# Performance work log

Hardware: AMD Instinct MI355X
Metric: run time of the kernel (lower is better)

The kernel has to match this reference:

```python
import jax, jax.numpy as jnp
import numpy as np

NEG_SLOPE = 0.01  # nn.LeakyReLU default

def leaky_relu(x):
    return jnp.where(x >= 0, x, NEG_SLOPE * x)

def rgcn_conv(x, weight, root, bias, src, dst, edge_type, num_relations, num_nodes):
    """PyG RGCNConv with default mean aggregation.
    weight: [R, in, out], root: [in, out], bias: [out].
    out[i] = x[i] @ root + bias + sum_r mean_{edges e of type r with dst=i} (x[src_e] @ W_r)
    """
    out = x @ root + bias
    for r in range(num_relations):
        mask = (edge_type == r)
        h = x @ weight[r]                       # [N, out] transform once per relation
        msg = h[src] * mask[:, None].astype(x.dtype)   # [E, out], zeroed off-relation
        s = jax.ops.segment_sum(msg, dst, num_segments=num_nodes)
        cnt = jax.ops.segment_sum(mask.astype(x.dtype), dst, num_segments=num_nodes)
        out = out + s / jnp.maximum(cnt, 1.0)[:, None]
    return out

def setup_inputs() -> dict:
    key = jax.random.key(0)
    ks = jax.random.split(key, 16)
    N, E, IN, HID, OUT, R = 50000, 800000, 768, 256, 2, 2
    x = jax.random.normal(ks[0], (N, IN), dtype=jnp.float32)
    edge_index = jax.random.randint(ks[1], (2, E), 0, N, dtype=jnp.int64)
    edge_weight = jax.random.uniform(ks[2], (E,), dtype=jnp.float32)
    edge_type = jax.random.randint(ks[3], (E,), 0, R, dtype=jnp.int64)
    def lin(k, fin, fout):
        s = 1.0 / np.sqrt(fin)
        k1, k2 = jax.random.split(k)
        W = jax.random.uniform(k1, (fin, fout), minval=-s, maxval=s, dtype=jnp.float32)
        b = jax.random.uniform(k2, (fout,), minval=-s, maxval=s, dtype=jnp.float32)
        return W, b
    fc1_W, fc1_b = lin(ks[4], IN, IN)
    fc2_W, fc2_b = lin(ks[5], HID, HID)
    out_W, out_b = lin(ks[6], HID, OUT)
    g = 1.0 / np.sqrt(IN)
    r1_weight = jax.random.uniform(ks[7], (R, IN, HID), minval=-g, maxval=g, dtype=jnp.float32)
    r1_root = jax.random.uniform(ks[8], (IN, HID), minval=-g, maxval=g, dtype=jnp.float32)
    r1_bias = jnp.zeros((HID,), dtype=jnp.float32)
    g2 = 1.0 / np.sqrt(HID)
    r2_weight = jax.random.uniform(ks[9], (R, HID, HID), minval=-g2, maxval=g2, dtype=jnp.float32)
    r2_root = jax.random.uniform(ks[10], (HID, HID), minval=-g2, maxval=g2, dtype=jnp.float32)
    r2_bias = jnp.zeros((HID,), dtype=jnp.float32)
    return {"x": x, "edge_index": edge_index, "edge_weight": edge_weight,
            "edge_type": edge_type,
            "fc1_W": fc1_W, "fc1_b": fc1_b,
            "r1_weight": r1_weight, "r1_root": r1_root, "r1_bias": r1_bias,
            "r2_weight": r2_weight, "r2_root": r2_root, "r2_bias": r2_bias,
            "fc2_W": fc2_W, "fc2_b": fc2_b,
            "out_W": out_W, "out_b": out_b}

def reference(x, edge_index, edge_weight, edge_type,
              fc1_W, fc1_b, r1_weight, r1_root, r1_bias,
              r2_weight, r2_root, r2_bias, fc2_W, fc2_b, out_W, out_b):
    N = x.shape[0]
    R = r1_weight.shape[0]
    src, dst = edge_index[0], edge_index[1]
    h = leaky_relu(x @ fc1_W + fc1_b)
    h = rgcn_conv(h, r1_weight, r1_root, r1_bias, src, dst, edge_type, R, N)
    h = rgcn_conv(h, r2_weight, r2_root, r2_bias, src, dst, edge_type, R, N)
    h = leaky_relu(h @ fc2_W + fc2_b)
    return jax.nn.softmax(h @ out_W + out_b, axis=1)
```

## Files before the change

### kernel.cpp

```cpp
#include <hip/hip_runtime.h>
#include <stdint.h>

__device__ __forceinline__ float b2f(unsigned short s) {
    union { uint32_t u; float f; } v; v.u = ((uint32_t)s) << 16; return v.f;
}
__device__ __forceinline__ unsigned short f2b(float f) {
    union { float f; uint32_t u; } v; v.f = f;
    uint32_t r = v.u + 0x7FFFu + ((v.u >> 16) & 1u);
    return (unsigned short)(r >> 16);
}
__device__ __forceinline__ int ld_idx(const void* p, long long i, int i64) {
    return i64 ? (int)((const long long*)p)[i] : ((const int*)p)[i];
}

typedef __bf16 bf16x8 __attribute__((ext_vector_type(8)));
typedef float  f32x4  __attribute__((ext_vector_type(4)));

__global__ void detect_kernel(const void* __restrict__ x, const void* __restrict__ eidx,
                              int* __restrict__ flags) {
    __shared__ int cntF, cntI;
    int t = threadIdx.x;
    if (t == 0) { cntF = 0; cntI = 0; }
    __syncthreads();
    const unsigned short* xs = (const unsigned short*)x;
    int lf = 0;
    for (int i = t; i < 4096; i += 256) {
        unsigned short v = xs[2 * i];
        int e = (v >> 7) & 0xFF;
        if (v == 0 || (e >= 100 && e <= 140)) lf++;
    }
    const int* ei = (const int*)eidx;
    int li = 0;
    for (int i = t; i < 2048; i += 256)
        if (ei[2 * i + 1] != 0) li++;
    atomicAdd(&cntF, lf);
    atomicAdd(&cntI, li);
    __syncthreads();
    if (t == 0) {
        flags[0] = (cntF < 3000) ? 1 : 0;
        flags[1] = (cntI < 64) ? 1 : 0;
    }
}

__global__ void convt_kernel(const void* __restrict__ W, size_t src_off,
                             unsigned short* __restrict__ Wt, int K, int N,
                             const int* __restrict__ flags) {
    int id = blockIdx.x * 256 + threadIdx.x;
    if (id < K * N) {
        int n = id / K, k = id - n * K;
        size_t s = src_off + (size_t)k * N + n;
        Wt[id] = flags[0] ? f2b(((const float*)W)[s]) : ((const unsigned short*)W)[s];
    }
}

__global__ void convb_kernel(const void* __restrict__ src, unsigned short* __restrict__ dst,
                             int n, const int* __restrict__ flags) {
    int i = blockIdx.x * 256 + threadIdx.x;
    if (i < n)
        dst[i] = flags[0] ? f2b(((const float*)src)[i]) : ((const unsigned short*)src)[i];
}

__global__ void convx_kernel(const void* __restrict__ src, unsigned short* __restrict__ dst,
                             int n8, const int* __restrict__ flags) {
    int i = blockIdx.x * 256 + threadIdx.x;
    if (i < n8) {
        if (flags[0]) {
            const float4* p = (const float4*)src + (size_t)i * 2;
            float4 a = p[0], b = p[1];
            union { int4 v; unsigned short s[8]; } u;
            u.s[0] = f2b(a.x); u.s[1] = f2b(a.y); u.s[2] = f2b(a.z); u.s[3] = f2b(a.w);
            u.s[4] = f2b(b.x); u.s[5] = f2b(b.y); u.s[6] = f2b(b.z); u.s[7] = f2b(b.w);
            ((int4*)dst)[i] = u.v;
        } else {
            ((int4*)dst)[i] = ((const int4*)src)[i];
        }
    }
}

__global__ void zero_kernel(int* __restrict__ p, int n) {
    int i = blockIdx.x * 256 + threadIdx.x;
    if (i < n) p[i] = 0;
}
__global__ void zero_us_kernel(unsigned short* __restrict__ p, int n) {
    int i = blockIdx.x * 256 + threadIdx.x;
    if (i < n) p[i] = 0;
}

__global__ void count_kernel(const void* __restrict__ eidx, const void* __restrict__ etype,
                             int* __restrict__ cnt, int E, int NN,
                             const int* __restrict__ flags) {
    int e = blockIdx.x * 256 + threadIdx.x;
    if (e < E) {
        int i64 = flags[1];
        int d = ld_idx(eidx, (long long)E + e, i64);
        d = min(max(d, 0), NN - 1);
        int ty = ld_idx(etype, e, i64) & 1;
        atomicAdd(&cnt[ty * NN + d], 1);
    }
}

__global__ void inv_deg_kernel(const int* __restrict__ cnt, float* __restrict__ inv,
                               int* __restrict__ deg, int NN) {
    int i = blockIdx.x * 256 + threadIdx.x;
    if (i < NN) {
        int c0 = cnt[i], c1 = cnt[NN + i];
        inv[i]      = 1.0f / (float)max(c0, 1);
        inv[NN + i] = 1.0f / (float)max(c1, 1);
        deg[i] = c0 + c1;
    }
}

__global__ void blocksum_kernel(const int* __restrict__ deg, int* __restrict__ bsum, int n) {
    __shared__ int red[256];
    int t = threadIdx.x, b = blockIdx.x;
    int base = b * 1024 + t * 4;
    int s = 0;
    #pragma unroll
    for (int j = 0; j < 4; ++j) {
        int idx = base + j;
        if (idx < n) s += deg[idx];
    }
    red[t] = s;
    __syncthreads();
    for (int off = 128; off > 0; off >>= 1) {
        if (t < off) red[t] += red[t + off];
        __syncthreads();
    }
    if (t == 0) bsum[b] = red[0];
}
__global__ void scan_bsum_kernel(int* __restrict__ bsum, int nb) {
    if (threadIdx.x == 0 && blockIdx.x == 0) {
        int acc = 0;
        for (int i = 0; i < nb; ++i) { int v = bsum[i]; bsum[i] = acc; acc += v; }
    }
}
__global__ void scan_phase3(const int* __restrict__ deg, const int* __restrict__ bsum,
                            int* __restrict__ row_ptr, int* __restrict__ pos, int n) {
    __shared__ int buf[256];
    int t = threadIdx.x, b = blockIdx.x;
    int base = b * 1024;
    int v[4]; int s = 0;
    #pragma unroll
    for (int j = 0; j < 4; ++j) {
        int idx = base + t * 4 + j;
        v[j] = (idx < n) ? deg[idx] : 0;
        s += v[j];
    }
    buf[t] = s;
    __syncthreads();
    for (int off = 1; off < 256; off <<= 1) {
        int xv = (t >= off) ? buf[t - off] : 0;
        __syncthreads();
        buf[t] += xv;
        __syncthreads();
    }
    int run = buf[t] - s + bsum[b];
    #pragma unroll
    for (int j = 0; j < 4; ++j) {
        int idx = base + t * 4 + j;
        if (idx < n) {
            run += v[j];
            row_ptr[idx + 1] = run;
            if (idx + 1 < n) pos[idx + 1] = run;
        }
    }
    if (b == 0 && t == 0) { row_ptr[0] = 0; pos[0] = 0; }
}

__global__ void fill_kernel(const void* __restrict__ eidx, const void* __restrict__ etype,
                            int* __restrict__ pos, int* __restrict__ packed, int E, int NN,
                            const int* __restrict__ flags) {
    int e = blockIdx.x * 256 + threadIdx.x;
    if (e < E) {
        int i64 = flags[1];
        int s = ld_idx(eidx, e, i64);
        int d = ld_idx(eidx, (long long)E + e, i64);
        s = min(max(s, 0), NN - 1);
        d = min(max(d, 0), NN - 1);
        int ty = ld_idx(etype, e, i64) & 1;
        int slot = atomicAdd(&pos[d], 1);
        packed[slot] = (ty << 24) | s;
    }
}

template<bool LEAKY, bool HAS_BIAS>
__global__ __launch_bounds__(256) void gemm_kernel(
    const unsigned short* __restrict__ A,
    const unsigned short* __restrict__ Wt,
    const unsigned short* __restrict__ bias,
    unsigned short* __restrict__ C,
    int M, int N, int K)
{
    __shared__ __align__(16) unsigned short As[128][72];
    __shared__ __align__(16) unsigned short Bs[128][72];

    const int t    = threadIdx.x;
    const int lane = t & 63;
    const int wave = t >> 6;
    const int wm   = wave >> 1;
    const int wn   = wave & 1;
    const int l16  = lane & 15;
    const int quad = lane >> 4;
    const int col0 = blockIdx.x * 128;
    const int row0 = blockIdx.y * 128;

    f32x4 acc[4][4] = {};

    for (int k0 = 0; k0 < K; k0 += 64) {
        #pragma unroll
        for (int i = 0; i < 4; ++i) {
            int c = t + 256 * i;
            int r = c >> 3, col = (c & 7) * 8;
            int gr = row0 + r;
            int4 v = make_int4(0, 0, 0, 0);
            if (gr < M)
                v = *reinterpret_cast<const int4*>(A + (size_t)gr * K + k0 + col);
            *reinterpret_cast<int4*>(&As[r][col]) = v;
        }
        #pragma unroll
        for (int i = 0; i < 4; ++i) {
            int c = t + 256 * i;
            int r = c >> 3, col = (c & 7) * 8;
            int4 v = *reinterpret_cast<const int4*>(&Wt[(size_t)(col0 + r) * K + k0 + col]);
            *reinterpret_cast<int4*>(&Bs[r][col]) = v;
        }
        __syncthreads();

        #pragma unroll
        for (int kk = 0; kk < 2; ++kk) {
            bf16x8 af[4], bfr[4];
            #pragma unroll
            for (int mi = 0; mi < 4; ++mi)
                af[mi] = *reinterpret_cast<const bf16x8*>(
                    &As[wm * 64 + mi * 16 + l16][kk * 32 + quad * 8]);
            #pragma unroll
            for (int ni = 0; ni < 4; ++ni)
                bfr[ni] = *reinterpret_cast<const bf16x8*>(
                    &Bs[wn * 64 + ni * 16 + l16][kk * 32 + quad * 8]);
            #pragma unroll
            for (int mi = 0; mi < 4; ++mi)
                #pragma unroll
                for (int ni = 0; ni < 4; ++ni)
                    acc[mi][ni] = __builtin_amdgcn_mfma_f32_16x16x32_bf16(
                        af[mi], bfr[ni], acc[mi][ni], 0, 0, 0);
        }
        __syncthreads();
    }

    #pragma unroll
    for (int mi = 0; mi < 4; ++mi) {
        #pragma unroll
        for (int ni = 0; ni < 4; ++ni) {
            int ccol = col0 + wn * 64 + ni * 16 + l16;
            float bv = HAS_BIAS ? b2f(bias[ccol]) : 0.0f;
            #pragma unroll
            for (int i = 0; i < 4; ++i) {
                int r = row0 + wm * 64 + mi * 16 + quad * 4 + i;
                if (r < M) {
                    float v = acc[mi][ni][i] + bv;
                    if (LEAKY) v = (v >= 0.0f) ? v : 0.01f * v;
                    C[(size_t)r * N + ccol] = f2b(v);
                }
            }
        }
    }
}

__global__ __launch_bounds__(256) void gather_kernel(
    const int* __restrict__ row_ptr, const int* __restrict__ packed,
    const float* __restrict__ inv,
    const unsigned short* __restrict__ P,
    unsigned short* __restrict__ outp,
    int NN)
{
    int i    = blockIdx.x * 4 + (threadIdx.x >> 6);
    int lane = threadIdx.x & 63;
    int half = lane >> 5;
    int l32  = lane & 31;
    if (i >= NN) return;
    float w0 = inv[i], w1 = inv[NN + i];
    float a[8] = {};
    if (half == 0) {
        union { int4 v; unsigned short s[8]; } ru;
        ru.v = *reinterpret_cast<const int4*>(P + (size_t)i * 768 + 512 + l32 * 8);
        #pragma unroll
        for (int j = 0; j < 8; ++j) a[j] = b2f(ru.s[j]);
    }
    int e1 = row_ptr[i + 1];
    for (int e = row_ptr[i] + half; e < e1; e += 2) {
        int p = packed[e];
        int s = p & 0xFFFFFF;
        if (s >= NN) s = NN - 1;
        int r = (p >> 24) & 1;
        float w = r ? w1 : w0;
        union { int4 v; unsigned short s8[8]; } hu;
        hu.v = *reinterpret_cast<const int4*>(P + (size_t)s * 768 + r * 256 + l32 * 8);
        #pragma unroll
        for (int j = 0; j < 8; ++j) a[j] += w * b2f(hu.s8[j]);
    }
    union { int4 v; unsigned short s[8]; } ou;
    #pragma unroll
    for (int j = 0; j < 8; ++j) {
        float m = a[j] + __shfl_down(a[j], 32);
        ou.s[j] = f2b(m);
    }
    if (half == 0)
        *reinterpret_cast<int4*>(outp + (size_t)i * 256 + l32 * 8) = ou.v;
}

__global__ __launch_bounds__(256) void head_kernel(
    const unsigned short* __restrict__ h,
    const unsigned short* __restrict__ outW,
    const unsigned short* __restrict__ outb,
    void* __restrict__ out, int M, const int* __restrict__ flags)
{
    int row  = blockIdx.x * 4 + (threadIdx.x >> 6);
    int lane = threadIdx.x & 63;
    if (row >= M) return;
    ushort4 hv = *reinterpret_cast<const ushort4*>(h + (size_t)row * 256 + lane * 4);
    union { int4 v; unsigned short s[8]; } wu;
    wu.v = *reinterpret_cast<const int4*>(outW + lane * 8);
    float hf[4] = { b2f(hv.x), b2f(hv.y), b2f(hv.z), b2f(hv.w) };
    float s0 = 0.0f, s1 = 0.0f;
    #pragma unroll
    for (int i = 0; i < 4; ++i) {
        s0 += hf[i] * b2f(wu.s[2 * i]);
        s1 += hf[i] * b2f(wu.s[2 * i + 1]);
    }
    #pragma unroll
    for (int off2 = 32; off2 >= 1; off2 >>= 1) {
        s0 += __shfl_down(s0, off2);
        s1 += __shfl_down(s1, off2);
    }
    if (lane == 0) {
        s0 += b2f(outb[0]); s1 += b2f(outb[1]);
        float m  = fmaxf(s0, s1);
        float e0 = expf(s0 - m), e1 = expf(s1 - m);
        float is = 1.0f / (e0 + e1);
        if (flags[0]) {
            ((float*)out)[(size_t)row * 2 + 0] = e0 * is;
            ((float*)out)[(size_t)row * 2 + 1] = e1 * is;
        } else {
            ((unsigned short*)out)[(size_t)row * 2 + 0] = f2b(e0 * is);
            ((unsigned short*)out)[(size_t)row * 2 + 1] = f2b(e1 * is);
        }
    }
}

__global__ void diag_kernel(unsigned short* __restrict__ out, int n, float v) {
    int i = blockIdx.x * 256 + threadIdx.x;
    if (i < n) out[i] = f2b(v);
}

template<bool LEAKY, bool HAS_BIAS>
static void launch_gemm(const unsigned short* A, const unsigned short* Wt,
                        const unsigned short* bias, unsigned short* C,
                        int M, int N, int K, hipStream_t s) {
    int MP = (M + 127) & ~127;
    dim3 grid(N / 128, MP / 128);
    gemm_kernel<LEAKY, HAS_BIAS><<<grid, 256, 0, s>>>(A, Wt, bias, C, M, N, K);
}

extern "C" void kernel_launch(void* const* d_in, const int* in_sizes, int n_in,
                              void* d_out, int out_size, void* d_ws, size_t ws_size,
                              hipStream_t stream) {
    const int IN = 768, HID = 256;
    const int NN = in_sizes[0] / IN;
    const int E  = in_sizes[3];
    const int MP = (NN + 127) & ~127;
    const int NB = (NN + 1023) / 1024;
    (void)n_in;

    const void* x    = d_in[0];
    const void* eidx = d_in[1];
    const void* etyp = d_in[3];
    const void* fc1W = d_in[4];
    const void* fc1b = d_in[5];
    const void* r1w  = d_in[6];
    const void* r1r  = d_in[7];
    const void* r1b  = d_in[8];
    const void* r2w  = d_in[9];
    const void* r2r  = d_in[10];
    const void* r2b  = d_in[11];
    const void* fc2W = d_in[12];
    const void* fc2b = d_in[13];
    const void* outW = d_in[14];
    const void* outb = d_in[15];

    char* ws = (char*)d_ws;
    size_t off = 0;
    auto carve = [&](size_t bytes) {
        char* p = ws + off; off += (bytes + 255) & ~(size_t)255; return p;
    };
    int*   flags = (int*)carve(64);
    unsigned short* fc1t  = (unsigned short*)carve((size_t)IN * IN * 2);
    unsigned short* Wcat1 = (unsigned short*)carve((size_t)IN * IN * 2);
    unsigned short* Wcat2 = (unsigned short*)carve((size_t)IN * HID * 2);
    unsigned short* fc2t  = (unsigned short*)carve((size_t)HID * HID * 2);
    unsigned short* fc1bc = (unsigned short*)carve((size_t)IN * 2);
    unsigned short* bcat1 = (unsigned short*)carve((size_t)IN * 2);
    unsigned short* bcat2 = (unsigned short*)carve((size_t)IN * 2);
    unsigned short* fc2bc = (unsigned short*)carve((size_t)HID * 2);
    unsigned short* outWc = (unsigned short*)carve((size_t)HID * 2 * 2);
    unsigned short* outbc = (unsigned short*)carve(2 * 2);
    int*   icnt    = (int*)carve((size_t)2 * NN * 4);
    float* inv     = (float*)carve((size_t)2 * NN * 4);
    int*   deg     = (int*)carve((size_t)NN * 4);
    int*   row_ptr = (int*)carve((size_t)(NN + 1) * 4);
    int*   pos     = (int*)carve((size_t)NN * 4);
    int*   bsum    = (int*)carve(256 * 4);
    int*   packed  = (int*)carve((size_t)E * 4);
    unsigned short* RA = (unsigned short*)carve((size_t)MP * IN * 2);
    unsigned short* RB = (unsigned short*)carve((size_t)MP * IN * 2);

    auto tg = [](int n) { return (n + 255) / 256; };

    if (ws_size < off) {
        float v = fminf((float)(ws_size >> 20), 300.0f) / 1000.0f;
        diag_kernel<<<tg(out_size), 256, 0, stream>>>((unsigned short*)d_out, out_size, v);
        return;
    }

    detect_kernel<<<1, 256, 0, stream>>>(x, eidx, flags);

    convt_kernel<<<tg(IN * IN), 256, 0, stream>>>(fc1W, 0, fc1t, IN, IN, flags);
    convt_kernel<<<tg(IN * HID), 256, 0, stream>>>(r1w, 0, Wcat1, IN, HID, flags);
    convt_kernel<<<tg(IN * HID), 256, 0, stream>>>(r1w, (size_t)IN * HID, Wcat1 + (size_t)256 * IN, IN, HID, flags);
    convt_kernel<<<tg(IN * HID), 256, 0, stream>>>(r1r, 0, Wcat1 + (size_t)512 * IN, IN, HID, flags);
    convt_kernel<<<tg(HID * HID), 256, 0, stream>>>(r2w, 0, Wcat2, HID, HID, flags);
    convt_kernel<<<tg(HID * HID), 256, 0, stream>>>(r2w, (size_t)HID * HID, Wcat2 + (size_t)256 * HID, HID, HID, flags);
    convt_kernel<<<tg(HID * HID), 256, 0, stream>>>(r2r, 0, Wcat2 + (size_t)512 * HID, HID, HID, flags);
    convt_kernel<<<tg(HID * HID), 256, 0, stream>>>(fc2W, 0, fc2t, HID, HID, flags);
    zero_us_kernel<<<tg(512), 256, 0, stream>>>(bcat1, 512);
    zero_us_kernel<<<tg(512), 256, 0, stream>>>(bcat2, 512);
    convb_kernel<<<tg(IN), 256, 0, stream>>>(fc1b, fc1bc, IN, flags);
    convb_kernel<<<1, 256, 0, stream>>>(r1b, bcat1 + 512, HID, flags);
    convb_kernel<<<1, 256, 0, stream>>>(r2b, bcat2 + 512, HID, flags);
    convb_kernel<<<1, 256, 0, stream>>>(fc2b, fc2bc, HID, flags);
    convb_kernel<<<tg(HID * 2), 256, 0, stream>>>(outW, outWc, HID * 2, flags);
    convb_kernel<<<1, 256, 0, stream>>>(outb, outbc, 2, flags);

    zero_kernel<<<tg(2 * NN), 256, 0, stream>>>(icnt, 2 * NN);
    count_kernel<<<tg(E), 256, 0, stream>>>(eidx, etyp, icnt, E, NN, flags);
    inv_deg_kernel<<<tg(NN), 256, 0, stream>>>(icnt, inv, deg, NN);
    blocksum_kernel<<<NB, 256, 0, stream>>>(deg, bsum, NN);
    scan_bsum_kernel<<<1, 64, 0, stream>>>(bsum, NB);
    scan_phase3<<<NB, 256, 0, stream>>>(deg, bsum, row_ptr, pos, NN);
    fill_kernel<<<tg(E), 256, 0, stream>>>(eidx, etyp, pos, packed, E, NN, flags);

    convx_kernel<<<tg(NN * IN / 8), 256, 0, stream>>>(x, RA, NN * IN / 8, flags);

    launch_gemm<true, true>(RA, fc1t, fc1bc, RB, NN, IN, IN, stream);

    launch_gemm<false, true>(RB, Wcat1, bcat1, RA, NN, IN, IN, stream);
    gather_kernel<<<(NN + 3) / 4, 256, 0, stream>>>(row_ptr, packed, inv, RA, RB, NN);

    launch_gemm<false, true>(RB, Wcat2, bcat2, RA, NN, IN, HID, stream);
    gather_kernel<<<(NN + 3) / 4, 256, 0, stream>>>(row_ptr, packed, inv, RA, RB, NN);

    launch_gemm<true, true>(RB, fc2t, fc2bc, RA, NN, HID, HID, stream);
    head_kernel<<<(NN + 3) / 4, 256, 0, stream>>>(RA, outWc, outbc, d_out, NN, flags);
}
```

Baseline: 871.0 us.

## Load GEMM B tile via direct global-to-LDS and widen gather edge parallelism

The GEMM's weight tile now goes from global memory straight into an unpadded LDS buffer through global_load_lds, so it no longer passes through registers. In the gather kernel each wave now covers four edges at once, 16 lanes per edge with 32-byte loads, followed by a two-step shuffle reduction. This is meant to raise memory-level parallelism in the irregular neighbor gather and to cut register traffic in the GEMM. The unpadded B layout may add LDS bank conflicts, and the gather holds more registers per thread.

Result: no change. 883.9 us (+1.5%).

```diff
diff --git a/kernel.cpp b/kernel.cpp
--- a/kernel.cpp
+++ b/kernel.cpp
@@ -192,7 +192,7 @@
     int M, int N, int K)
 {
     __shared__ __align__(16) unsigned short As[128][72];
-    __shared__ __align__(16) unsigned short Bs[128][72];
+    __shared__ __align__(16) unsigned short Bs[128 * 64];
 
     const int t    = threadIdx.x;
     const int lane = t & 63;
@@ -203,10 +203,21 @@
     const int quad = lane >> 4;
     const int col0 = blockIdx.x * 128;
     const int row0 = blockIdx.y * 128;
+    const int srow = wave * 8 + (lane >> 3);
+    const int scol = (lane & 7) * 8;
 
     f32x4 acc[4][4] = {};
 
     for (int k0 = 0; k0 < K; k0 += 64) {
+        #pragma unroll
+        for (int j = 0; j < 4; ++j) {
+            __builtin_amdgcn_global_load_lds(
+                (const __attribute__((address_space(1))) unsigned int*)
+                    (Wt + (size_t)(col0 + j * 32 + srow) * K + k0 + scol),
+                (__attribute__((address_space(3))) unsigned int*)
+                    (&Bs[(j * 32 + wave * 8) * 64]),
+                16, 0, 0);
+        }
         #pragma unroll
         for (int i = 0; i < 4; ++i) {
             int c = t + 256 * i;
@@ -216,13 +227,6 @@
             if (gr < M)
                 v = *reinterpret_cast<const int4*>(A + (size_t)gr * K + k0 + col);
             *reinterpret_cast<int4*>(&As[r][col]) = v;
-        }
-        #pragma unroll
-        for (int i = 0; i < 4; ++i) {
-            int c = t + 256 * i;
-            int r = c >> 3, col = (c & 7) * 8;
-            int4 v = *reinterpret_cast<const int4*>(&Wt[(size_t)(col0 + r) * K + k0 + col]);
-            *reinterpret_cast<int4*>(&Bs[r][col]) = v;
         }
         __syncthreads();
 
@@ -236,7 +240,7 @@
             #pragma unroll
             for (int ni = 0; ni < 4; ++ni)
                 bfr[ni] = *reinterpret_cast<const bf16x8*>(
-                    &Bs[wn * 64 + ni * 16 + l16][kk * 32 + quad * 8]);
+                    &Bs[(wn * 64 + ni * 16 + l16) * 64 + kk * 32 + quad * 8]);
             #pragma unroll
             for (int mi = 0; mi < 4; ++mi)
                 #pragma unroll
@@ -275,37 +279,47 @@
 {
     int i    = blockIdx.x * 4 + (threadIdx.x >> 6);
     int lane = threadIdx.x & 63;
-    int half = lane >> 5;
-    int l32  = lane & 31;
+    int q    = lane >> 4;
+    int l16  = lane & 15;
     if (i >= NN) return;
     float w0 = inv[i], w1 = inv[NN + i];
-    float a[8] = {};
-    if (half == 0) {
-        union { int4 v; unsigned short s[8]; } ru;
-        ru.v = *reinterpret_cast<const int4*>(P + (size_t)i * 768 + 512 + l32 * 8);
-        #pragma unroll
-        for (int j = 0; j < 8; ++j) a[j] = b2f(ru.s[j]);
+    float a[16] = {};
+    if (q == 0) {
+        const int4* rp = (const int4*)(P + (size_t)i * 768 + 512 + l16 * 16);
+        union { int4 v; unsigned short s[8]; } r0u, r1u;
+        r0u.v = rp[0]; r1u.v = rp[1];
+        #pragma unroll
+        for (int j = 0; j < 8; ++j) { a[j] = b2f(r0u.s[j]); a[8 + j] = b2f(r1u.s[j]); }
     }
     int e1 = row_ptr[i + 1];
-    for (int e = row_ptr[i] + half; e < e1; e += 2) {
+    for (int e = row_ptr[i] + q; e < e1; e += 4) {
         int p = packed[e];
         int s = p & 0xFFFFFF;
         if (s >= NN) s = NN - 1;
         int r = (p >> 24) & 1;
         float w = r ? w1 : w0;
-        union { int4 v; unsigned short s8[8]; } hu;
-        hu.v = *reinterpret_cast<const int4*>(P + (size_t)s * 768 + r * 256 + l32 * 8);
-        #pragma unroll
-        for (int j = 0; j < 8; ++j) a[j] += w * b2f(hu.s8[j]);
-    }
-    union { int4 v; unsigned short s[8]; } ou;
-    #pragma unroll
-    for (int j = 0; j < 8; ++j) {
-        float m = a[j] + __shfl_down(a[j], 32);
-        ou.s[j] = f2b(m);
-    }
-    if (half == 0)
-        *reinterpret_cast<int4*>(outp + (size_t)i * 256 + l32 * 8) = ou.v;
+        const int4* hp = (const int4*)(P + (size_t)s * 768 + r * 256 + l16 * 16);
+        union { int4 v; unsigned short s8[8]; } h0, h1;
+        h0.v = hp[0]; h1.v = hp[1];
+        #pragma unroll
+        for (int j = 0; j < 8; ++j) {
+            a[j]     += w * b2f(h0.s8[j]);
+            a[8 + j] += w * b2f(h1.s8[j]);
+        }
+    }
+    #pragma unroll
+    for (int j = 0; j < 16; ++j) {
+        a[j] += __shfl_down(a[j], 32);
+        a[j] += __shfl_down(a[j], 16);
+    }
+    if (q == 0) {
+        union { int4 v; unsigned short s[8]; } o0, o1;
+        #pragma unroll
+        for (int j = 0; j < 8; ++j) { o0.s[j] = f2b(a[j]); o1.s[j] = f2b(a[8 + j]); }
+        int4* op = (int4*)(outp + (size_t)i * 256 + l16 * 16);
+        op[0] = o0.v;
+        op[1] = o1.v;
+    }
 }
 
 __global__ __launch_bounds__(256) void head_kernel(
```
